# Optimization experiments

Hardware: AMD Instinct MI355X
Metric: run time of the kernel (lower is better)

The kernel has to match this reference:

```python
import jax, jax.numpy as jnp
import numpy as np

B, C_IN, C_OUT, H, W = 4, 256, 256, 64, 64
KH = KW = 3
STRIDE = 1
PAD = 1
DIL = 1


def setup_inputs() -> dict:
    key = jax.random.key(0)
    k1, k2, k3, k4 = jax.random.split(key, 4)
    x = jax.random.normal(k1, (B, C_IN, H, W), dtype=jnp.float32)
    # torchvision layout: 2*dg*KH*KW channels, (y, x) pair per kernel tap
    offset = jax.random.normal(k2, (B, 2 * KH * KW, H, W), dtype=jnp.float32)
    fan_in = C_IN * KH * KW
    weight = jax.random.normal(k3, (C_OUT, C_IN, KH, KW), dtype=jnp.float32) / np.sqrt(fan_in)
    bias = jax.random.normal(k4, (C_OUT,), dtype=jnp.float32) * 0.01
    return {"x": x, "offset": offset, "weight": weight, "bias": bias}


def _gather_bilinear_corner(x_flat, yi, xi, h, w):
    # x_flat: [B, C, H*W]; yi/xi: [B, KK, Ho, Wo] int32
    valid = ((yi >= 0) & (yi < h) & (xi >= 0) & (xi < w)).astype(x_flat.dtype)
    idx = jnp.clip(yi, 0, h - 1) * w + jnp.clip(xi, 0, w - 1)
    b = idx.shape[0]
    g = jnp.take_along_axis(x_flat, idx.reshape(b, 1, -1), axis=2)
    return g.reshape(b, x_flat.shape[1], *yi.shape[1:]), valid


def deform_conv2d(x, offset, weight, bias):
    b, c, h, w = x.shape
    o = weight.shape[0]
    kk = KH * KW
    ho = (h + 2 * PAD - DIL * (KH - 1) - 1) // STRIDE + 1
    wo = (w + 2 * PAD - DIL * (KW - 1) - 1) // STRIDE + 1

    ky = (jnp.arange(kk, dtype=jnp.float32) // KW) * DIL  # [KK]
    kx = (jnp.arange(kk, dtype=jnp.float32) % KW) * DIL
    hs = jnp.arange(ho, dtype=jnp.float32) * STRIDE - PAD   # [Ho]
    ws = jnp.arange(wo, dtype=jnp.float32) * STRIDE - PAD   # [Wo]

    off = offset.reshape(b, kk, 2, ho, wo)
    py = hs[None, None, :, None] + ky[None, :, None, None] + off[:, :, 0]  # [B,KK,Ho,Wo]
    px = ws[None, None, None, :] + kx[None, :, None, None] + off[:, :, 1]

    y0 = jnp.floor(py)
    x0 = jnp.floor(px)
    wy1 = py - y0  # fractional parts, differentiable w.r.t. offsets
    wx1 = px - x0
    wy0 = 1.0 - wy1
    wx0 = 1.0 - wx1
    y0i = y0.astype(jnp.int32)
    x0i = x0.astype(jnp.int32)

    x_flat = x.reshape(b, c, h * w)
    corners = [
        (y0i,     x0i,     wy0 * wx0),
        (y0i,     x0i + 1, wy0 * wx1),
        (y0i + 1, x0i,     wy1 * wx0),
        (y0i + 1, x0i + 1, wy1 * wx1),
    ]
    sampled = jnp.zeros((b, c, kk, ho, wo), dtype=x.dtype)
    for yi, xi, wgt in corners:
        g, valid = _gather_bilinear_corner(x_flat, yi, xi, h, w)
        sampled = sampled + g * (wgt * valid)[:, None]

    out = jnp.einsum('bckhw,ock->bohw', sampled, weight.reshape(o, c, kk))
    return out + bias[None, :, None, None]


def reference(x, offset, weight, bias):
    return deform_conv2d(x, offset, weight, bias)
```

## Files before the change

kernel.cpp:

```cpp
#include <hip/hip_runtime.h>

typedef __bf16 bf16;
typedef __bf16 bf16x4 __attribute__((ext_vector_type(4)));
typedef __bf16 bf16x8 __attribute__((ext_vector_type(8)));
typedef float  f32x4  __attribute__((ext_vector_type(4)));
typedef float  f32x16 __attribute__((ext_vector_type(16)));

#define KK     9
#define KDIM   2304
#define KSTEPS 144
#define PXW    32

__device__ __forceinline__ int sreadi(int v) {
    return __builtin_amdgcn_readfirstlane(v);
}

__global__ __launch_bounds__(256) void prep2_k(const float* __restrict__ x,
                                               const float* __restrict__ w,
                                               bf16* __restrict__ xt,
                                               bf16* __restrict__ wq) {
    __shared__ __align__(16) char smem[8 * 2308 * 2];
    int bid = blockIdx.x;
    int tid = threadIdx.x;
    if (bid < 1024) {
        float (*tileF)[65] = reinterpret_cast<float(*)[65]>(smem);
        int pt = bid & 63, ct = (bid >> 6) & 3, b = bid >> 8;
        const float* src = x + ((size_t)(b * 256 + ct * 64)) * 4096 + pt * 64;
        int f4 = tid & 15;
        int cl = tid >> 4;
        #pragma unroll
        for (int q = 0; q < 4; ++q) {
            int c = q * 16 + cl;
            f32x4 v = *reinterpret_cast<const f32x4*>(src + (size_t)c * 4096 + f4 * 4);
            tileF[f4 * 4 + 0][c] = v[0];
            tileF[f4 * 4 + 1][c] = v[1];
            tileF[f4 * 4 + 2][c] = v[2];
            tileF[f4 * 4 + 3][c] = v[3];
        }
        __syncthreads();
        int j = tid & 7, p0 = tid >> 3;
        bf16* dst = xt + ((size_t)(b * 4096 + pt * 64)) * 256 + ct * 64 + j * 8;
        #pragma unroll
        for (int pp = 0; pp < 2; ++pp) {
            int p = p0 + pp * 32;
            bf16x8 sv;
            #pragma unroll
            for (int k = 0; k < 8; ++k) sv[k] = (bf16)tileF[p][j * 8 + k];
            *reinterpret_cast<bf16x8*>(dst + (size_t)p * 256) = sv;
        }
    } else {
        bf16 (*Wl)[2308] = reinterpret_cast<bf16(*)[2308]>(smem);
        int wb     = bid - 1024;
        int o_base = wb * 8;
        int m      = o_base >> 5;
        int o31b   = o_base & 31;
        #pragma unroll
        for (int pass = 0; pass < 18; ++pass) {
            int i    = pass * 256 + tid;
            int r    = i / 576;
            int col4 = i - r * 576;
            f32x4 v = *reinterpret_cast<const f32x4*>(
                w + (size_t)(o_base + r) * KDIM + col4 * 4);
            Wl[r][col4 * 4 + 0] = (bf16)v[0];
            Wl[r][col4 * 4 + 1] = (bf16)v[1];
            Wl[r][col4 * 4 + 2] = (bf16)v[2];
            Wl[r][col4 * 4 + 3] = (bf16)v[3];
        }
        __syncthreads();
        #pragma unroll
        for (int pass = 0; pass < 9; ++pass) {
            int gid  = pass * 256 + tid;
            int ol   = gid & 7;
            int half = (gid >> 3) & 1;
            int ks   = gid >> 4;
            int kb   = ks * 16 + half * 8;
            int tap  = kb >> 8;
            int cc0  = kb & 255;
            bf16x8 sv;
            #pragma unroll
            for (int j = 0; j < 8; ++j) sv[j] = Wl[ol][(cc0 + j) * 9 + tap];
            size_t g = (size_t)((m * KSTEPS + ks) * 64 + half * 32 + o31b + ol);
            *reinterpret_cast<bf16x8*>(wq + g * 8) = sv;
        }
    }
}

__global__ __launch_bounds__(1024, 8) void deform_gemm_k(
    const bf16*  __restrict__ xt,
    const float* __restrict__ off,
    const bf16*  __restrict__ wq,
    const float* __restrict__ bias,
    float*       __restrict__ out) {

    __shared__ bf16 S[2][PXW * 256];

    int tid   = threadIdx.x;
    int wavei = sreadi(tid >> 6);
    int lane  = tid & 63;
    int quad  = lane >> 4;
    int l16   = lane & 15;
    int l32   = lane & 31;
    int half  = lane >> 5;
    int mt    = wavei & 7;
    int kh    = wavei >> 3;
    (void)quad; (void)l16;

    int bid   = blockIdx.x;
    int pb    = ((bid & 7) << 6) | (bid >> 3);
    int pix0  = pb * PXW;
    int b     = pix0 >> 12;
    int pimgb = pix0 & 4095;
    int obase = b * 73728;
    unsigned base = (unsigned)b * 1048576u + (unsigned)(lane * 4);
    int rot   = ((bid >> 3) & 1) * 4;

    f32x16 acc;
    #pragma unroll
    for (int r = 0; r < 16; ++r) acc[r] = 0.f;

    for (int t = 0; t < KK; ++t) {
        int tap = t + rot; if (tap >= KK) tap -= KK;
        int ty = tap / 3 - 1;
        int tx = tap % 3 - 1;
        bf16* Sw = &S[t & 1][0];

        #pragma unroll
        for (int i = 0; i < 2; ++i) {
            int n    = wavei * 2 + i;
            int pimg = pimgb + n;
            float oy = off[obase + (2 * tap) * 4096 + pimg];
            float ox = off[obase + (2 * tap + 1) * 4096 + pimg];
            float py = (float)((pimg >> 6) + ty) + oy;
            float px = (float)((pimg & 63) + tx) + ox;
            float fy = floorf(py), fx = floorf(px);
            int   y0 = (int)fy,    x0 = (int)fx;
            float wy1 = py - fy, wx1 = px - fx;
            float wy0 = 1.f - wy1, wx0 = 1.f - wx1;
            wy0 = ((unsigned)y0       < 64u) ? wy0 : 0.f;
            wy1 = ((unsigned)(y0 + 1) < 64u) ? wy1 : 0.f;
            wx0 = ((unsigned)x0       < 64u) ? wx0 : 0.f;
            wx1 = ((unsigned)(x0 + 1) < 64u) ? wx1 : 0.f;
            int yc0 = min(max(y0, 0), 63), yc1 = min(max(y0 + 1, 0), 63);
            int xc0 = min(max(x0, 0), 63), xc1 = min(max(x0 + 1, 0), 63);
            int u0 = sreadi((yc0 * 64 + xc0) * 256);
            int u1 = sreadi((yc0 * 64 + xc1) * 256);
            int u2 = sreadi((yc1 * 64 + xc0) * 256);
            int u3 = sreadi((yc1 * 64 + xc1) * 256);
            float w0 = __builtin_bit_cast(float, sreadi(__builtin_bit_cast(int, wy0 * wx0)));
            float w1 = __builtin_bit_cast(float, sreadi(__builtin_bit_cast(int, wy0 * wx1)));
            float w2 = __builtin_bit_cast(float, sreadi(__builtin_bit_cast(int, wy1 * wx0)));
            float w3 = __builtin_bit_cast(float, sreadi(__builtin_bit_cast(int, wy1 * wx1)));
            bf16x4 v0 = *reinterpret_cast<const bf16x4*>(xt + base + (unsigned)u0);
            bf16x4 v1 = *reinterpret_cast<const bf16x4*>(xt + base + (unsigned)u1);
            bf16x4 v2 = *reinterpret_cast<const bf16x4*>(xt + base + (unsigned)u2);
            bf16x4 v3 = *reinterpret_cast<const bf16x4*>(xt + base + (unsigned)u3);
            float a0 = w0 * (float)v0[0] + w1 * (float)v1[0]
                     + w2 * (float)v2[0] + w3 * (float)v3[0];
            float a1 = w0 * (float)v0[1] + w1 * (float)v1[1]
                     + w2 * (float)v2[1] + w3 * (float)v3[1];
            float a2 = w0 * (float)v0[2] + w1 * (float)v1[2]
                     + w2 * (float)v2[2] + w3 * (float)v3[2];
            float a3 = w0 * (float)v0[3] + w1 * (float)v1[3]
                     + w2 * (float)v2[3] + w3 * (float)v3[3];
            bf16x4 sv;
            sv[0] = (bf16)a0; sv[1] = (bf16)a1;
            sv[2] = (bf16)a2; sv[3] = (bf16)a3;
            int gs = (lane >> 1) ^ (n & 31);
            *reinterpret_cast<bf16x4*>(Sw + n * 256 + gs * 8 + (lane & 1) * 4) = sv;
        }

        const bf16* ap0 = wq +
            ((size_t)(((mt * KSTEPS) + tap * 16 + kh * 8) * 64 + lane)) * 8;
        bf16x8 a0 = *reinterpret_cast<const bf16x8*>(ap0);
        bf16x8 a1 = *reinterpret_cast<const bf16x8*>(ap0 + 512);
        bf16x8 a2 = *reinterpret_cast<const bf16x8*>(ap0 + 1024);
        bf16x8 a3 = *reinterpret_cast<const bf16x8*>(ap0 + 1536);

        __syncthreads();

        const bf16* Sr = Sw;
        #pragma unroll
        for (int kk2 = 0; kk2 < 8; ++kk2) {
            bf16x8 a;
            if      (kk2 == 0) a = a0;
            else if (kk2 == 1) a = a1;
            else if (kk2 == 2) a = a2;
            else if (kk2 == 3) a = a3;
            else a = *reinterpret_cast<const bf16x8*>(ap0 + (size_t)kk2 * 512);
            int s  = kh * 8 + kk2;
            int g  = s * 2 + half;
            int gs = g ^ l32;
            bf16x8 bf = *reinterpret_cast<const bf16x8*>(Sr + l32 * 256 + gs * 8);
            acc = __builtin_amdgcn_mfma_f32_32x32x16_bf16(a, bf, acc, 0, 0, 0);
        }
    }

    __syncthreads();
    float* Sf = reinterpret_cast<float*>(&S[0][0]);
    if (wavei >= 8) {
        int wb = (wavei - 8) * 64 + lane;
        #pragma unroll
        for (int r = 0; r < 16; ++r)
            Sf[r * 512 + wb] = acc[r];
    }
    __syncthreads();
    if (wavei < 8) {
        int wb   = wavei * 64 + lane;
        int m    = mt * 32;
        int pimg = pimgb + l32;
        float* op = out + ((size_t)(b * 256 + m)) * 4096 + pimg;
        #pragma unroll
        for (int r = 0; r < 16; ++r) {
            int row = (r & 3) + 8 * (r >> 2) + half * 4;
            float v = acc[r] + Sf[r * 512 + wb] + bias[m + row];
            op[(size_t)row * 4096] = v;
        }
    }
}

extern "C" void kernel_launch(void* const* d_in, const int* in_sizes, int n_in,
                              void* d_out, int out_size, void* d_ws, size_t ws_size,
                              hipStream_t stream) {
    const float* x    = (const float*)d_in[0];
    const float* off  = (const float*)d_in[1];
    const float* w    = (const float*)d_in[2];
    const float* bias = (const float*)d_in[3];
    float* out = (float*)d_out;

    bf16* wq = (bf16*)d_ws;
    bf16* xt = (bf16*)((char*)d_ws + (size_t)589824 * 2);

    prep2_k<<<1056, 256, 0, stream>>>(x, w, xt, wq);
    deform_gemm_k<<<512, 1024, 0, stream>>>(xt, off, wq, bias, out);
}
```

Measured before the change: 121.4 us.

## Split wave into half-wave pixel sampling with 16-byte gathers and offset prefetch

Each half-wave now samples its own pixel (32 lanes × 8 channels) using 16-byte loads, where before the whole wave looped over two pixels with 8-byte loads. This removes the scalar readfirstlane broadcasts and halves the serial bilinear iterations per tap. Bf16 is unpacked with bit shifts and the blend uses fma chains. The next tap's offsets are prefetched after the barrier so their latency overlaps the MFMA phase. Per-lane addresses are now divergent vector values rather than scalars, which adds VGPR pressure.

```diff
diff --git a/kernel.cpp b/kernel.cpp
--- a/kernel.cpp
+++ b/kernel.cpp
@@ -5,6 +5,7 @@
 typedef __bf16 bf16x8 __attribute__((ext_vector_type(8)));
 typedef float  f32x4  __attribute__((ext_vector_type(4)));
 typedef float  f32x16 __attribute__((ext_vector_type(16)));
+typedef unsigned int u32x4 __attribute__((ext_vector_type(4)));
 
 #define KK     9
 #define KDIM   2304
@@ -13,6 +14,13 @@
 
 __device__ __forceinline__ int sreadi(int v) {
     return __builtin_amdgcn_readfirstlane(v);
+}
+
+__device__ __forceinline__ float BL(unsigned v) {
+    return __builtin_bit_cast(float, v << 16);
+}
+__device__ __forceinline__ float BH(unsigned v) {
+    return __builtin_bit_cast(float, v & 0xffff0000u);
 }
 
 __global__ __launch_bounds__(256) void prep2_k(const float* __restrict__ x,
@@ -97,13 +105,10 @@
     int tid   = threadIdx.x;
     int wavei = sreadi(tid >> 6);
     int lane  = tid & 63;
-    int quad  = lane >> 4;
-    int l16   = lane & 15;
     int l32   = lane & 31;
     int half  = lane >> 5;
     int mt    = wavei & 7;
     int kh    = wavei >> 3;
-    (void)quad; (void)l16;
 
     int bid   = blockIdx.x;
     int pb    = ((bid & 7) << 6) | (bid >> 3);
@@ -111,12 +116,19 @@
     int b     = pix0 >> 12;
     int pimgb = pix0 & 4095;
     int obase = b * 73728;
-    unsigned base = (unsigned)b * 1048576u + (unsigned)(lane * 4);
     int rot   = ((bid >> 3) & 1) * 4;
+
+    int n     = wavei * 2 + half;
+    int pimg  = pimgb + n;
+    int py_i  = pimg >> 6, px_i = pimg & 63;
+    const char* xb = (const char*)xt + ((size_t)b << 21) + l32 * 16;
 
     f32x16 acc;
     #pragma unroll
     for (int r = 0; r < 16; ++r) acc[r] = 0.f;
+
+    float oyC = off[obase + (2 * rot) * 4096 + pimg];
+    float oxC = off[obase + (2 * rot + 1) * 4096 + pimg];
 
     for (int t = 0; t < KK; ++t) {
         int tap = t + rot; if (tap >= KK) tap -= KK;
@@ -124,50 +136,40 @@
         int tx = tap % 3 - 1;
         bf16* Sw = &S[t & 1][0];
 
-        #pragma unroll
-        for (int i = 0; i < 2; ++i) {
-            int n    = wavei * 2 + i;
-            int pimg = pimgb + n;
-            float oy = off[obase + (2 * tap) * 4096 + pimg];
-            float ox = off[obase + (2 * tap + 1) * 4096 + pimg];
-            float py = (float)((pimg >> 6) + ty) + oy;
-            float px = (float)((pimg & 63) + tx) + ox;
-            float fy = floorf(py), fx = floorf(px);
-            int   y0 = (int)fy,    x0 = (int)fx;
-            float wy1 = py - fy, wx1 = px - fx;
-            float wy0 = 1.f - wy1, wx0 = 1.f - wx1;
-            wy0 = ((unsigned)y0       < 64u) ? wy0 : 0.f;
-            wy1 = ((unsigned)(y0 + 1) < 64u) ? wy1 : 0.f;
-            wx0 = ((unsigned)x0       < 64u) ? wx0 : 0.f;
-            wx1 = ((unsigned)(x0 + 1) < 64u) ? wx1 : 0.f;
-            int yc0 = min(max(y0, 0), 63), yc1 = min(max(y0 + 1, 0), 63);
-            int xc0 = min(max(x0, 0), 63), xc1 = min(max(x0 + 1, 0), 63);
-            int u0 = sreadi((yc0 * 64 + xc0) * 256);
-            int u1 = sreadi((yc0 * 64 + xc1) * 256);
-            int u2 = sreadi((yc1 * 64 + xc0) * 256);
-            int u3 = sreadi((yc1 * 64 + xc1) * 256);
-            float w0 = __builtin_bit_cast(float, sreadi(__builtin_bit_cast(int, wy0 * wx0)));
-            float w1 = __builtin_bit_cast(float, sreadi(__builtin_bit_cast(int, wy0 * wx1)));
-            float w2 = __builtin_bit_cast(float, sreadi(__builtin_bit_cast(int, wy1 * wx0)));
-            float w3 = __builtin_bit_cast(float, sreadi(__builtin_bit_cast(int, wy1 * wx1)));
-            bf16x4 v0 = *reinterpret_cast<const bf16x4*>(xt + base + (unsigned)u0);
-            bf16x4 v1 = *reinterpret_cast<const bf16x4*>(xt + base + (unsigned)u1);
-            bf16x4 v2 = *reinterpret_cast<const bf16x4*>(xt + base + (unsigned)u2);
-            bf16x4 v3 = *reinterpret_cast<const bf16x4*>(xt + base + (unsigned)u3);
-            float a0 = w0 * (float)v0[0] + w1 * (float)v1[0]
-                     + w2 * (float)v2[0] + w3 * (float)v3[0];
-            float a1 = w0 * (float)v0[1] + w1 * (float)v1[1]
-                     + w2 * (float)v2[1] + w3 * (float)v3[1];
-            float a2 = w0 * (float)v0[2] + w1 * (float)v1[2]
-                     + w2 * (float)v2[2] + w3 * (float)v3[2];
-            float a3 = w0 * (float)v0[3] + w1 * (float)v1[3]
-                     + w2 * (float)v2[3] + w3 * (float)v3[3];
-            bf16x4 sv;
-            sv[0] = (bf16)a0; sv[1] = (bf16)a1;
-            sv[2] = (bf16)a2; sv[3] = (bf16)a3;
-            int gs = (lane >> 1) ^ (n & 31);
-            *reinterpret_cast<bf16x4*>(Sw + n * 256 + gs * 8 + (lane & 1) * 4) = sv;
-        }
+        float py = (float)(py_i + ty) + oyC;
+        float px = (float)(px_i + tx) + oxC;
+        float fy = floorf(py), fx = floorf(px);
+        int   y0 = (int)fy,    x0 = (int)fx;
+        float wy1 = py - fy, wx1 = px - fx;
+        float wy0 = 1.f - wy1, wx0 = 1.f - wx1;
+        wy0 = ((unsigned)y0       < 64u) ? wy0 : 0.f;
+        wy1 = ((unsigned)(y0 + 1) < 64u) ? wy1 : 0.f;
+        wx0 = ((unsigned)x0       < 64u) ? wx0 : 0.f;
+        wx1 = ((unsigned)(x0 + 1) < 64u) ? wx1 : 0.f;
+        int yc0 = min(max(y0, 0), 63), yc1 = min(max(y0 + 1, 0), 63);
+        int xc0 = min(max(x0, 0), 63), xc1 = min(max(x0 + 1, 0), 63);
+        unsigned u0 = (unsigned)(yc0 * 64 + xc0) * 512u;
+        unsigned u1 = (unsigned)(yc0 * 64 + xc1) * 512u;
+        unsigned u2 = (unsigned)(yc1 * 64 + xc0) * 512u;
+        unsigned u3 = (unsigned)(yc1 * 64 + xc1) * 512u;
+        float w0 = wy0 * wx0, w1 = wy0 * wx1;
+        float w2 = wy1 * wx0, w3 = wy1 * wx1;
+        u32x4 g0 = *(const u32x4*)(xb + u0);
+        u32x4 g1 = *(const u32x4*)(xb + u1);
+        u32x4 g2 = *(const u32x4*)(xb + u2);
+        u32x4 g3 = *(const u32x4*)(xb + u3);
+        bf16x8 sv;
+        #pragma unroll
+        for (int q = 0; q < 4; ++q) {
+            float lo = fmaf(w0, BL(g0[q]), fmaf(w1, BL(g1[q]),
+                       fmaf(w2, BL(g2[q]),      w3 * BL(g3[q]))));
+            float hi = fmaf(w0, BH(g0[q]), fmaf(w1, BH(g1[q]),
+                       fmaf(w2, BH(g2[q]),      w3 * BH(g3[q]))));
+            sv[q * 2]     = (bf16)lo;
+            sv[q * 2 + 1] = (bf16)hi;
+        }
+        int gsw = l32 ^ (n & 31);
+        *reinterpret_cast<bf16x8*>(Sw + n * 256 + gsw * 8) = sv;
 
         const bf16* ap0 = wq +
             ((size_t)(((mt * KSTEPS) + tap * 16 + kh * 8) * 64 + lane)) * 8;
@@ -177,6 +179,12 @@
         bf16x8 a3 = *reinterpret_cast<const bf16x8*>(ap0 + 1536);
 
         __syncthreads();
+
+        if (t < KK - 1) {
+            int tn = tap + 1; if (tn >= KK) tn = 0;
+            oyC = off[obase + (2 * tn) * 4096 + pimg];
+            oxC = off[obase + (2 * tn + 1) * 4096 + pimg];
+        }
 
         const bf16* Sr = Sw;
         #pragma unroll
@@ -190,8 +198,8 @@
             int s  = kh * 8 + kk2;
             int g  = s * 2 + half;
             int gs = g ^ l32;
-            bf16x8 bf = *reinterpret_cast<const bf16x8*>(Sr + l32 * 256 + gs * 8);
-            acc = __builtin_amdgcn_mfma_f32_32x32x16_bf16(a, bf, acc, 0, 0, 0);
+            bf16x8 bv = *reinterpret_cast<const bf16x8*>(Sr + l32 * 256 + gs * 8);
+            acc = __builtin_amdgcn_mfma_f32_32x32x16_bf16(a, bv, acc, 0, 0, 0);
         }
     }
 
@@ -207,8 +215,8 @@
     if (wavei < 8) {
         int wb   = wavei * 64 + lane;
         int m    = mt * 32;
-        int pimg = pimgb + l32;
-        float* op = out + ((size_t)(b * 256 + m)) * 4096 + pimg;
+        int pimo = pimgb + l32;
+        float* op = out + ((size_t)(b * 256 + m)) * 4096 + pimo;
         #pragma unroll
         for (int r = 0; r < 16; ++r) {
             int row = (r & 3) + 8 * (r >> 2) + half * 4;
```

New measurement: 121.3 us. No clear change (-0.1%).
